# Optimization experiments

Hardware: AMD Instinct MI355X
Metric: run time of the kernel (lower is better)

## Reference

```python
import jax, jax.numpy as jnp
import numpy as np

B = 256
IN_CH = 1
E = 8          # embedding_channels (power of 2)
DEPTH = 3      # log2(E)
T = 8192       # time_range
WINDOW = 2.0
K = 15         # kernel_size (odd -> torch 'same' == lax 'SAME')
TPI = 2.0 * np.pi


def conv1d(x, w, b, dilation=1, groups=1):
    # x: (B, Cin, T), w: (Cout, Cin/groups, K), b: (Cout,)
    out = jax.lax.conv_general_dilated(
        x, w, window_strides=(1,), padding='SAME',
        rhs_dilation=(dilation,),
        dimension_numbers=('NCH', 'OIH', 'NCH'),
        feature_group_count=groups)
    return out + b[None, :, None]


def setup_inputs() -> dict:
    key = jax.random.key(0)
    ks = jax.random.split(key, 14)
    s = 0.05
    x = jax.random.normal(ks[0], (B, T), jnp.float32)
    W1 = jax.random.normal(ks[1], (E, 2, 1, K), jnp.float32) * s   # per-channel Conv1d(1,2)
    b1 = jax.random.normal(ks[2], (E, 2), jnp.float32) * s
    W2 = jax.random.normal(ks[3], (E, 1, 2, K), jnp.float32) * s   # per-channel Conv1d(2,1)
    b2 = jax.random.normal(ks[4], (E, 1), jnp.float32) * s
    fcW = jax.random.normal(ks[5], (E, 2, T), jnp.float32) * 0.01  # per-channel Linear(T, 2)
    fcb = jax.random.normal(ks[6], (E, 2), jnp.float32) * s
    # deconv tree: level j has 2**(DEPTH-1-j) Conv1d(2,1) units, stacked as grouped conv
    dW0 = jax.random.normal(ks[7], (4, 2, K), jnp.float32) * s
    db0 = jax.random.normal(ks[8], (4,), jnp.float32) * s
    dW1 = jax.random.normal(ks[9], (2, 2, K), jnp.float32) * s
    db1 = jax.random.normal(ks[10], (2,), jnp.float32) * s
    dW2 = jax.random.normal(ks[11], (1, 2, K), jnp.float32) * s
    db2 = jax.random.normal(ks[12], (1,), jnp.float32) * s
    return dict(x=x, W1=W1, b1=b1, W2=W2, b2=b2, fcW=fcW, fcb=fcb,
                dW0=dW0, db0=db0, dW1=dW1, db1=db1, dW2=dW2, db2=db2)


def reference(x, W1, b1, W2, b2, fcW, fcb, dW0, db0, dW1, db1, dW2, db2):
    y = x.reshape(x.shape[0], IN_CH, T)
    # per-channel dilated conv stack (dilation = 2**i)
    chans = []
    for i in range(E):
        h = conv1d(y, W1[i], b1[i], dilation=2 ** i)
        chans.append(conv1d(h, W2[i], b2[i], dilation=2 ** i))
    latent = jnp.concatenate(chans, axis=1)                # (B, E, T)
    # FFT -> frequency / amplitude / offset
    rfft = jnp.fft.rfft(latent, axis=2)                    # (B, E, T//2+1)
    power = jnp.abs(rfft[:, :, 1:]) ** 2
    freqs = jnp.asarray(np.fft.rfftfreq(T)[1:] * T / WINDOW, jnp.float32)
    psum = jnp.sum(power, axis=2)
    f = jnp.sum(freqs * power, axis=2) / psum              # (B, E)
    a = 2.0 * jnp.sqrt(psum) / T
    b_off = rfft.real[:, :, 0] / T
    # per-channel Linear(T, 2) -> phase
    v = jnp.einsum('bet,ect->bec', latent, fcW) + fcb      # (B, E, 2)
    p = jnp.arctan2(v[..., 1], v[..., 0]) / TPI            # (B, E)
    # sinusoid reconstruction
    args = jnp.linspace(-WINDOW / 2, WINDOW / 2, T, dtype=jnp.float32)
    sig = a[..., None] * jnp.sin(TPI * (f[..., None] * args + p[..., None])) + b_off[..., None]
    # deconv tree: pairs of channels -> grouped conv, halving channels each level
    y = sig
    for dW, db in ((dW0, db0), (dW1, db1), (dW2, db2)):
        y = conv1d(y, dW, db, dilation=1, groups=dW.shape[0])
    out = y.reshape(y.shape[0], IN_CH * T)
    return (out, latent, sig,
            p[..., None], f[..., None], a[..., None], b_off[..., None])
```

## Files before the change

### kernel.cpp

```cpp
#include <hip/hip_runtime.h>
#include <math.h>

#define TT 8192
#define BB 256
#define EE 8
#define KK 15
#define PI_F  3.14159265358979323846f
#define TPI_F 6.28318530717958647692f

#define OFF_OUT 0
#define OFF_LAT (BB*TT)
#define OFF_SIG (OFF_LAT + BB*EE*TT)
#define OFF_P   (OFF_SIG + BB*EE*TT)
#define OFF_F   (OFF_P + BB*EE)
#define OFF_A   (OFF_F + BB*EE)
#define OFF_B0  (OFF_A + BB*EE)

#define SWZ(i) ((i) + ((i) >> 5))
#define NF 4096

#define L_RE   0
#define L_IM   4223
#define L_SXP  8446
#define L_SW   16382
#define L_RBUF 16478
#define L_TOT  16510

__device__ __forceinline__ float rdfl(float v) {
  return __uint_as_float(__builtin_amdgcn_readfirstlane(__float_as_uint(v)));
}

__device__ __forceinline__ int rev4(int k) {
  unsigned r = __brev((unsigned)k) >> 20;
  return (int)(((r & 0x555u) << 1) | ((r >> 1) & 0x555u));
}

__global__ __launch_bounds__(512) void conv_fft_kernel(
    const float* __restrict__ x, const float* __restrict__ W1,
    const float* __restrict__ b1, const float* __restrict__ W2,
    const float* __restrict__ b2, const float* __restrict__ fcW,
    const float* __restrict__ fcb, float* __restrict__ latent,
    float* __restrict__ outP, float* __restrict__ outF,
    float* __restrict__ outA, float* __restrict__ outB0)
{
  extern __shared__ float smem[];
  float* re   = smem + L_RE;
  float* im   = smem + L_IM;
  float* sxp  = smem + L_SXP;
  float* sW   = smem + L_SW;
  float* rbuf = smem + L_RBUF;

  const int e = blockIdx.x, b = blockIdx.y;
  const int d  = 1 << e;
  const int Mh = (TT/2) >> e;
  const int Lp = ((((Mh - 2) + 31) >> 5) << 5) + 30;
  const int tid = threadIdx.x;
  const float* xr = x + b * TT;

  if (tid < 29) {
    float acc = 0.0f;
    for (int c = 0; c < 2; c++) {
      const float* w1 = W1 + e*30 + c*15;
      const float* w2 = W2 + e*30 + c*15;
      int jlo = tid - 14; if (jlo < 0) jlo = 0;
      int jhi = tid;      if (jhi > 14) jhi = 14;
      for (int j = jlo; j <= jhi; j++) acc += w2[j] * w1[tid - j];
    }
    sW[tid] = acc;
  } else if (tid == 29) {
    float s20 = 0.f, s21 = 0.f;
    for (int j = 0; j < 15; j++) { s20 += W2[e*30 + j]; s21 += W2[e*30 + 15 + j]; }
    sW[29] = b2[e] + s20*b1[e*2] + s21*b1[e*2 + 1];
  } else if (tid >= 32 && tid < 62) {
    sW[tid] = W1[e*30 + (tid - 32)];
  } else if (tid >= 64 && tid < 94) {
    sW[tid] = W2[e*30 + (tid - 64)];
  } else if (tid == 94 || tid == 95) {
    sW[tid] = b1[e*2 + (tid - 94)];
  }

  float Wc[29];
  float Bc = 0.0f;
  bool wloaded = false;

  #pragma unroll 1
  for (int h = 0; h < 2; ++h) {
    const int tbase = h * (TT/2) - 14 * d;
    const int nstage = (TT/2) + 28 * d;
    for (int i = tid; i < nstage; i += 512) {
      int t  = tbase + i;
      int ph = i & (d - 1);
      int n  = i >> e;
      sxp[ph * Lp + n] = (t >= 0 && t < TT) ? xr[t] : 0.0f;
    }
    __syncthreads();

    if (!wloaded) {
      #pragma unroll
      for (int s = 0; s < 29; s++) Wc[s] = rdfl(sW[s]);
      Bc = rdfl(sW[29]);
      wloaded = true;
    }

    float* lr = latent + (b * EE + e) * TT + h * (TT/2);

    #pragma unroll 1
    for (int g = 0; g < 2; g++) {
      const int vt = g * 512 + tid;
      const int ph = vt & (d - 1);
      const int m0 = (vt >> e) << 2;

      float win[32];
      {
        const float2* wp = (const float2*)&sxp[ph * Lp + m0];
        #pragma unroll
        for (int v = 0; v < 16; v++) {
          float2 qv = wp[v];
          win[2*v] = qv.x; win[2*v+1] = qv.y;
        }
      }
      float acc[4] = {Bc, Bc, Bc, Bc};
      #pragma unroll
      for (int s = 0; s < 29; s++) {
        #pragma unroll
        for (int r = 0; r < 4; r++) acc[r] = fmaf(Wc[s], win[s + r], acc[r]);
      }

      if (h == 0 && g == 0 && m0 <= 6) {
        #pragma unroll
        for (int r = 0; r < 4; r++) {
          float corr = 0.0f;
          #pragma unroll
          for (int j = 0; j < 7; j++) {
            if (m0 + r + j <= 6) {
              float a0 = sW[94], a1 = sW[95];
              #pragma unroll
              for (int k = 0; k < 15; k++) {
                float xv = win[r + j + k];
                a0 = fmaf(sW[32 + k], xv, a0);
                a1 = fmaf(sW[47 + k], xv, a1);
              }
              corr = fmaf(sW[64 + j], a0, corr);
              corr = fmaf(sW[79 + j], a1, corr);
            }
          }
          acc[r] -= corr;
        }
      }
      if (h == 1 && g == 1 && m0 + 3 >= Mh - 7) {
        #pragma unroll
        for (int r = 0; r < 4; r++) {
          float corr = 0.0f;
          #pragma unroll
          for (int jj = 0; jj < 7; jj++) {
            const int j = 8 + jj;
            if (m0 + r + j >= Mh + 7) {
              float a0 = sW[94], a1 = sW[95];
              #pragma unroll
              for (int k = 0; k < 15; k++) {
                float xv = win[r + j + k];
                a0 = fmaf(sW[32 + k], xv, a0);
                a1 = fmaf(sW[47 + k], xv, a1);
              }
              corr = fmaf(sW[64 + j], a0, corr);
              corr = fmaf(sW[79 + j], a1, corr);
            }
          }
          acc[r] -= corr;
        }
      }

      #pragma unroll
      for (int r = 0; r < 4; r++) {
        int toff = ph + (m0 + r) * d;
        lr[toff] = acc[r];
        int tg = h * (TT/2) + toff;
        int n  = tg >> 1;
        float* dst = (tg & 1) ? im : re;
        dst[SWZ(n)] = acc[r];
      }
    }
    __syncthreads();
  }

  const float2* f02 = (const float2*)(fcW + (e*2 + 0)*TT);
  const float2* f12 = (const float2*)(fcW + (e*2 + 1)*TT);
  float v0 = 0.f, v1 = 0.f;
  for (int n = tid; n < NF; n += 512) {
    float zr = re[SWZ(n)], zi = im[SWZ(n)];
    float2 a0 = f02[n], a1 = f12[n];
    v0 = fmaf(zr, a0.x, v0); v0 = fmaf(zi, a0.y, v0);
    v1 = fmaf(zr, a1.x, v1); v1 = fmaf(zi, a1.y, v1);
  }
  __syncthreads();

  for (int L = NF >> 2; L >= 1; L >>= 2) {
    float wstep = -1.57079632679f / (float)L;
    for (int u = tid; u < (NF >> 2); u += 512) {
      int p = u & (L - 1);
      int base = ((u - p) << 2) + p;
      int i0 = SWZ(base), i1 = SWZ(base + L), i2 = SWZ(base + 2*L), i3 = SWZ(base + 3*L);
      float ar = re[i0], ai = im[i0];
      float br = re[i1], bi = im[i1];
      float cr = re[i2], ci = im[i2];
      float dr = re[i3], di = im[i3];
      float t0r = ar + cr, t0i = ai + ci;
      float t1r = ar - cr, t1i = ai - ci;
      float t2r = br + dr, t2i = bi + di;
      float t3r = br - dr, t3i = bi - di;
      float A0r = t0r + t2r, A0i = t0i + t2i;
      float A1r = t1r + t3i, A1i = t1i - t3r;
      float A2r = t0r - t2r, A2i = t0i - t2i;
      float A3r = t1r - t3i, A3i = t1i + t3r;
      float ang = wstep * (float)p;
      float s1 = __sinf(ang), c1 = __cosf(ang);
      float c2 = c1*c1 - s1*s1, s2 = 2.f*c1*s1;
      float c3 = c1*c2 - s1*s2, s3 = c1*s2 + s1*c2;
      re[i0] = A0r;                 im[i0] = A0i;
      re[i1] = A1r*c1 - A1i*s1;     im[i1] = A1r*s1 + A1i*c1;
      re[i2] = A2r*c2 - A2i*s2;     im[i2] = A2r*s2 + A2i*c2;
      re[i3] = A3r*c3 - A3i*s3;     im[i3] = A3r*s3 + A3i*c3;
    }
    __syncthreads();
  }

  float pacc = 0.f, facc = 0.f;
  for (int k = 1 + tid; k < NF; k += 512) {
    int jk = SWZ(rev4(k));
    int jm = SWZ(rev4(NF - k));
    float zr = re[jk], zi = im[jk];
    float yr = re[jm], yi = im[jm];
    float Er = 0.5f*(zr + yr), Ei = 0.5f*(zi - yi);
    float Dr = 0.5f*(zr - yr), Di = 0.5f*(zi + yi);
    float Or = Di, Oi = -Dr;
    float ang = -PI_F * (float)k / (float)NF;
    float s = __sinf(ang), c = __cosf(ang);
    float Xr = Er + c*Or - s*Oi;
    float Xi = Ei + c*Oi + s*Or;
    float mag = fmaf(Xr, Xr, Xi*Xi);
    pacc += mag;
    facc = fmaf(0.5f * (float)k, mag, facc);
  }
  if (tid == 0) {
    float X = re[SWZ(0)] - im[SWZ(0)];
    pacc += X*X;
    facc += 2048.0f * X*X;
  }

  #pragma unroll
  for (int off = 32; off > 0; off >>= 1) {
    pacc += __shfl_down(pacc, off);
    facc += __shfl_down(facc, off);
    v0   += __shfl_down(v0, off);
    v1   += __shfl_down(v1, off);
  }
  int wid = tid >> 6, lane = tid & 63;
  if (lane == 0) {
    rbuf[wid*4 + 0] = pacc; rbuf[wid*4 + 1] = facc;
    rbuf[wid*4 + 2] = v0;   rbuf[wid*4 + 3] = v1;
  }
  __syncthreads();
  if (tid == 0) {
    float P = 0.f, Fw = 0.f, V0 = 0.f, V1 = 0.f;
    #pragma unroll
    for (int w = 0; w < 8; w++) {
      P += rbuf[w*4]; Fw += rbuf[w*4+1]; V0 += rbuf[w*4+2]; V1 += rbuf[w*4+3];
    }
    float z0r = re[SWZ(0)], z0i = im[SWZ(0)];
    float amp  = 2.0f * sqrtf(P) / (float)TT;
    float boff = (z0r + z0i) / (float)TT;
    float vv0 = V0 + fcb[e*2 + 0];
    float vv1 = V1 + fcb[e*2 + 1];
    float ph  = atan2f(vv1, vv0) / TPI_F;
    int idx = b*EE + e;
    outP[idx]  = ph;
    outF[idx]  = Fw / P;
    outA[idx]  = amp;
    outB0[idx] = boff;
  }
}

#define TILE_C 512
#define SST 556
#define SL0 544
#define SL1 528

__global__ __launch_bounds__(256) void sig_deconv_kernel(
    const float* __restrict__ Pv, const float* __restrict__ Fv,
    const float* __restrict__ Av, const float* __restrict__ B0v,
    const float* __restrict__ dW0, const float* __restrict__ db0,
    const float* __restrict__ dW1, const float* __restrict__ db1,
    const float* __restrict__ dW2, const float* __restrict__ db2,
    float* __restrict__ sig, float* __restrict__ out)
{
  __shared__ float smem[4*SL0 + 8*SST];
  float* sl0  = smem;
  float* ssig = smem + 4*SL0;
  float* sl1  = smem + 4*SL0;

  const int tile = blockIdx.x, b = blockIdx.y;
  const int t0 = tile * TILE_C;
  const int tid = threadIdx.x;
  const float step = 2.0f / 8191.0f;

  float fs[8], am[8], psh[8], bo[8];
  #pragma unroll
  for (int ch = 0; ch < EE; ch++) {
    int idx = b*EE + ch;
    fs[ch] = Fv[idx]; am[ch] = Av[idx]; psh[ch] = Pv[idx]; bo[ch] = B0v[idx];
  }

  for (int i = tid; i < SST; i += 256) {
    int t = t0 + i - 21;
    bool in = (i < 554 && t >= 0 && t < TT);
    float arg = fmaf(step, (float)t, -1.0f);
    bool wr = (i >= 21 && i < 21 + TILE_C);
    #pragma unroll
    for (int ch = 0; ch < EE; ch++) {
      float rr = fmaf(fs[ch], arg, psh[ch]);
      rr -= rintf(rr);
      float val = in ? fmaf(am[ch], __sinf(TPI_F * rr), bo[ch]) : 0.0f;
      ssig[ch*SST + i] = val;
      if (wr) sig[(b*EE + ch)*TT + t] = val;
    }
  }
  __syncthreads();

  for (int g = 0; g < 4; g++) {
    float bg = db0[g];
    for (int u = tid; u < 135; u += 256) {
      const float4* p0 = (const float4*)(ssig + (2*g)*SST + 4*u);
      const float4* p1 = (const float4*)(ssig + (2*g+1)*SST + 4*u);
      float w0[20], w1[20];
      #pragma unroll
      for (int v = 0; v < 5; v++) {
        float4 q0 = p0[v], q1 = p1[v];
        w0[4*v]=q0.x; w0[4*v+1]=q0.y; w0[4*v+2]=q0.z; w0[4*v+3]=q0.w;
        w1[4*v]=q1.x; w1[4*v+1]=q1.y; w1[4*v+2]=q1.z; w1[4*v+3]=q1.w;
      }
      #pragma unroll
      for (int r = 0; r < 4; r++) {
        int i0 = 4*u + r;
        int t = t0 + i0 - 14;
        float a2 = bg;
        #pragma unroll
        for (int k = 0; k < KK; k++) {
          a2 = fmaf(dW0[g*30 + k],      w0[r + k], a2);
          a2 = fmaf(dW0[g*30 + 15 + k], w1[r + k], a2);
        }
        sl0[g*SL0 + i0] = (t >= 0 && t < TT) ? a2 : 0.0f;
      }
    }
  }
  if (tid < 16) sl0[(tid >> 2)*SL0 + 540 + (tid & 3)] = 0.0f;
  __syncthreads();

  for (int g = 0; g < 2; g++) {
    float bg = db1[g];
    for (int u = tid; u < 132; u += 256) {
      const float4* p0 = (const float4*)(sl0 + (2*g)*SL0 + 4*u);
      const float4* p1 = (const float4*)(sl0 + (2*g+1)*SL0 + 4*u);
      float w0[20], w1[20];
      #pragma unroll
      for (int v = 0; v < 5; v++) {
        float4 q0 = p0[v], q1 = p1[v];
        w0[4*v]=q0.x; w0[4*v+1]=q0.y; w0[4*v+2]=q0.z; w0[4*v+3]=q0.w;
        w1[4*v]=q1.x; w1[4*v+1]=q1.y; w1[4*v+2]=q1.z; w1[4*v+3]=q1.w;
      }
      #pragma unroll
      for (int r = 0; r < 4; r++) {
        int i1 = 4*u + r;
        if (i1 < 526) {
          int t = t0 + i1 - 7;
          float a2 = bg;
          #pragma unroll
          for (int k = 0; k < KK; k++) {
            a2 = fmaf(dW1[g*30 + k],      w0[r + k], a2);
            a2 = fmaf(dW1[g*30 + 15 + k], w1[r + k], a2);
          }
          sl1[g*SL1 + i1] = (t >= 0 && t < TT) ? a2 : 0.0f;
        }
      }
    }
  }
  __syncthreads();

  if (tid < 128) {
    float bg = db2[0];
    float* orow = out + b*TT + t0;
    int u = tid;
    const float4* p0 = (const float4*)(sl1 + 4*u);
    const float4* p1 = (const float4*)(sl1 + SL1 + 4*u);
    float w0[20], w1[20];
    #pragma unroll
    for (int v = 0; v < 5; v++) {
      float4 q0 = p0[v], q1 = p1[v];
      w0[4*v]=q0.x; w0[4*v+1]=q0.y; w0[4*v+2]=q0.z; w0[4*v+3]=q0.w;
      w1[4*v]=q1.x; w1[4*v+1]=q1.y; w1[4*v+2]=q1.z; w1[4*v+3]=q1.w;
    }
    float4 res;
    float* resf = (float*)&res;
    #pragma unroll
    for (int r = 0; r < 4; r++) {
      float a2 = bg;
      #pragma unroll
      for (int k = 0; k < KK; k++) {
        a2 = fmaf(dW2[k],      w0[r + k], a2);
        a2 = fmaf(dW2[15 + k], w1[r + k], a2);
      }
      resf[r] = a2;
    }
    ((float4*)orow)[u] = res;
  }
}

extern "C" void kernel_launch(void* const* d_in, const int* in_sizes, int n_in,
                              void* d_out, int out_size, void* d_ws, size_t ws_size,
                              hipStream_t stream) {
  const float* x   = (const float*)d_in[0];
  const float* W1  = (const float*)d_in[1];
  const float* b1  = (const float*)d_in[2];
  const float* W2  = (const float*)d_in[3];
  const float* b2  = (const float*)d_in[4];
  const float* fcW = (const float*)d_in[5];
  const float* fcb = (const float*)d_in[6];
  const float* dW0 = (const float*)d_in[7];
  const float* db0 = (const float*)d_in[8];
  const float* dW1 = (const float*)d_in[9];
  const float* db1 = (const float*)d_in[10];
  const float* dW2 = (const float*)d_in[11];
  const float* db2 = (const float*)d_in[12];

  float* o        = (float*)d_out;
  float* out_main = o + OFF_OUT;
  float* latent   = o + OFF_LAT;
  float* sig      = o + OFF_SIG;
  float* pP  = o + OFF_P;
  float* pF  = o + OFF_F;
  float* pA  = o + OFF_A;
  float* pB0 = o + OFF_B0;

  const size_t lds_fused = L_TOT * sizeof(float);
  conv_fft_kernel<<<dim3(EE, BB), 512, lds_fused, stream>>>(
      x, W1, b1, W2, b2, fcW, fcb, latent, pP, pF, pA, pB0);
  sig_deconv_kernel<<<dim3(TT/TILE_C, BB), 256, 0, stream>>>(
      pP, pF, pA, pB0, dW0, db0, dW1, db1, dW2, db2, sig, out_main);
}
```

Baseline: 343.7 us.

## Compute interior deconv tiles analytically via sinusoid frequency response

Result: no change. 345.9 us (+0.7%).

```diff
diff --git a/kernel.cpp b/kernel.cpp
--- a/kernel.cpp
+++ b/kernel.cpp
@@ -294,9 +294,6 @@
     float* __restrict__ sig, float* __restrict__ out)
 {
   __shared__ float smem[4*SL0 + 8*SST];
-  float* sl0  = smem;
-  float* ssig = smem + 4*SL0;
-  float* sl1  = smem + 4*SL0;
 
   const int tile = blockIdx.x, b = blockIdx.y;
   const int t0 = tile * TILE_C;
@@ -309,6 +306,91 @@
     int idx = b*EE + ch;
     fs[ch] = Fv[idx]; am[ch] = Av[idx]; psh[ch] = Pv[idx]; bo[ch] = B0v[idx];
   }
+
+  if (tile >= 1 && tile <= 14) {
+    float* hre   = smem;
+    float* him   = smem + 24;
+    float* ssum  = smem + 48;
+    float* Cs    = smem + 72;
+    float* Cc    = smem + 80;
+    float* chDC  = smem + 88;
+    float* bDC   = smem + 96;
+
+    if (tid < 24) {
+      int ch  = tid & 7;
+      int lvl = tid >> 3;
+      const float* w;
+      if (lvl == 0)      w = dW0 + (ch >> 1)*30 + (ch & 1)*15;
+      else if (lvl == 1) w = dW1 + (ch >> 2)*30 + ((ch >> 1) & 1)*15;
+      else               w = dW2 + (ch >> 2)*15;
+      float om = TPI_F * fs[ch] * step;
+      float ar = 0.f, ai = 0.f, sm = 0.f;
+      #pragma unroll
+      for (int k = 0; k < 15; k++) {
+        float wk = w[k];
+        float ang = (float)(k - 7) * om;
+        ar = fmaf(wk, __cosf(ang), ar);
+        ai = fmaf(wk, __sinf(ang), ai);
+        sm += wk;
+      }
+      hre[tid] = ar; him[tid] = ai; ssum[tid] = sm;
+    }
+    __syncthreads();
+
+    if (tid < 8) {
+      int ch = tid;
+      float r0 = hre[ch],      i0 = him[ch];
+      float r1 = hre[8 + ch],  i1 = him[8 + ch];
+      float r2 = hre[16 + ch], i2 = him[16 + ch];
+      float ra = r0*r1 - i0*i1, ia = r0*i1 + i0*r1;
+      float rt = ra*r2 - ia*i2, it = ra*i2 + ia*r2;
+      Cs[ch] = am[ch] * rt;
+      Cc[ch] = am[ch] * it;
+      chDC[ch] = bo[ch] * ssum[ch] * ssum[8 + ch] * ssum[16 + ch];
+    } else if (tid == 8) {
+      float acc = db2[0];
+      #pragma unroll
+      for (int g0 = 0; g0 < 4; g0++)
+        acc = fmaf(db0[g0], ssum[8 + 2*g0] * ssum[16 + 2*g0], acc);
+      #pragma unroll
+      for (int g1 = 0; g1 < 2; g1++)
+        acc = fmaf(db1[g1], ssum[16 + 4*g1], acc);
+      bDC[0] = acc;
+    }
+    __syncthreads();
+
+    float cs[8], cc[8];
+    float DC = bDC[0];
+    #pragma unroll
+    for (int ch = 0; ch < 8; ch++) {
+      cs[ch] = Cs[ch]; cc[ch] = Cc[ch]; DC += chDC[ch];
+    }
+
+    float* orow = out + b*TT;
+    #pragma unroll
+    for (int it = 0; it < 2; ++it) {
+      int t = t0 + it*256 + tid;
+      float arg = fmaf(step, (float)t, -1.0f);
+      float o = DC;
+      #pragma unroll
+      for (int ch = 0; ch < 8; ch++) {
+        float rr = fmaf(fs[ch], arg, psh[ch]);
+        rr -= rintf(rr);
+        float th = TPI_F * rr;
+        float s = __sinf(th);
+        float c = __cosf(th);
+        sig[(b*EE + ch)*TT + t] = fmaf(am[ch], s, bo[ch]);
+        o = fmaf(s, cs[ch], o);
+        o = fmaf(c, cc[ch], o);
+      }
+      orow[t] = o;
+    }
+    return;
+  }
+
+  float* sl0  = smem;
+  float* ssig = smem + 4*SL0;
+  float* sl1  = smem + 4*SL0;
 
   for (int i = tid; i < SST; i += 256) {
     int t = t0 + i - 21;
```
